# Kernel tuning notes

Measured on AMD Instinct MI355X. Metric: run time of the kernel, lower is better.

## Reference

```python
import jax, jax.numpy as jnp
import numpy as np

B, S, K, D = 2, 2048, 8, 1024
P, KP, DFF = 32, 4, 4096


def setup_inputs() -> dict:
    key = jax.random.key(0)
    ks = jax.random.split(key, 17)
    s = 0.02
    return {
        "x": jax.random.normal(ks[0], (B, S, D), jnp.float32),
        "router_out": jax.random.normal(ks[1], (B, S, D), jnp.float32),
        "topk_neuron_idx": jax.random.randint(ks[2], (B, S, K), 0, 512, jnp.int32),
        "topk_neuron_weights": jax.random.uniform(ks[3], (B, S, K), jnp.float32),
        "selected_neurons": jax.random.normal(ks[4], (B, S, K, D), jnp.float32),
        "context": jax.random.normal(ks[5], (B, S, D), jnp.float32),
        "Wq": jax.random.normal(ks[6], (D, D), jnp.float32) * s,
        "bq": jnp.zeros((D,), jnp.float32),
        "Wk": jax.random.normal(ks[7], (D, D), jnp.float32) * s,
        "bk": jnp.zeros((D,), jnp.float32),
        "Wv": jax.random.normal(ks[8], (D, D), jnp.float32) * s,
        "bv": jnp.zeros((D,), jnp.float32),
        "pattern_queries": jax.random.normal(ks[9], (P, D), jnp.float32) * s,
        "Wup": jax.random.normal(ks[10], (DFF, D), jnp.float32) * s,
        "bup": jnp.zeros((DFF,), jnp.float32),
        "Wdown": jax.random.normal(ks[11], (D, DFF), jnp.float32) * s,
        "bdown": jnp.zeros((D,), jnp.float32),
    }


def reference(x, router_out, topk_neuron_idx, topk_neuron_weights,
              selected_neurons, context, Wq, bq, Wk, bk, Wv, bv,
              pattern_queries, Wup, bup, Wdown, bdown):
    scale = 1.0 / jnp.sqrt(jnp.float32(D))
    # K-wide neuron self-attention (per token), torch Linear: y = x @ W.T + b
    q = jnp.einsum('bskd,ed->bske', selected_neurons, Wq) + bq
    kk = jnp.einsum('bskd,ed->bske', selected_neurons, Wk) + bk
    v = jnp.einsum('bskd,ed->bske', selected_neurons, Wv) + bv
    attn = jax.nn.softmax(jnp.einsum('bsqd,bskd->bsqk', q, kk) * scale, axis=-1)
    interacted = jnp.einsum('bsqk,bskd->bsqd', attn, v)  # [B,S,K,D]
    # pattern similarity: [B,S,P,K]
    nps = jnp.einsum('pd,bskd->bspk', pattern_queries, interacted) * scale
    neuron_based = (nps * topk_neuron_weights[:, :, None, :]).sum(-1)  # [B,S,P]
    context_based = jnp.einsum('bsd,pd->bsp', context, pattern_queries)
    pattern_scores = 0.5 * neuron_based + 0.5 * context_based
    topk_scores, topk_idx = jax.lax.top_k(pattern_scores, KP)  # [B,S,KP]
    topk_w = jax.nn.softmax(topk_scores, axis=-1)
    sel_attn = jnp.take_along_axis(nps, topk_idx[..., None], axis=2)  # [B,S,KP,K]
    final_attn = (topk_w[..., None] * jax.nn.softmax(sel_attn, axis=-1)).sum(2)  # [B,S,K]
    aggregated = jnp.einsum('bsk,bskd->bsd', final_attn, interacted)
    combined = x + aggregated
    h = jax.nn.gelu(combined @ Wup.T + bup, approximate=False)
    return h @ Wdown.T + bdown
```

## Files before the change

### kernel.cpp

```cpp
#include <hip/hip_runtime.h>
#include <math.h>

typedef unsigned short ushort_t;
typedef __attribute__((ext_vector_type(8))) short short8;
typedef __attribute__((ext_vector_type(4))) float floatx4;

static __device__ __forceinline__ ushort_t f2bf(float f){
  unsigned int u = __float_as_uint(f);
  unsigned int r = u + 0x7FFFu + ((u >> 16) & 1u);
  return (ushort_t)(r >> 16);
}
static __device__ __forceinline__ void unpack8(uint4 u, float* f){
  f[0] = __uint_as_float(u.x << 16); f[1] = __uint_as_float(u.x & 0xffff0000u);
  f[2] = __uint_as_float(u.y << 16); f[3] = __uint_as_float(u.y & 0xffff0000u);
  f[4] = __uint_as_float(u.z << 16); f[5] = __uint_as_float(u.z & 0xffff0000u);
  f[6] = __uint_as_float(u.w << 16); f[7] = __uint_as_float(u.w & 0xffff0000u);
}
static __device__ __forceinline__ uint4 pack8(const float* f){
  uint4 u;
  u.x = (unsigned)f2bf(f[0]) | ((unsigned)f2bf(f[1]) << 16);
  u.y = (unsigned)f2bf(f[2]) | ((unsigned)f2bf(f[3]) << 16);
  u.z = (unsigned)f2bf(f[4]) | ((unsigned)f2bf(f[5]) << 16);
  u.w = (unsigned)f2bf(f[6]) | ((unsigned)f2bf(f[7]) << 16);
  return u;
}

static __device__ __forceinline__ void gload16(const void* g, void* l){
  __builtin_amdgcn_global_load_lds((const __attribute__((address_space(1))) void*)g,
                                   (__attribute__((address_space(3))) void*)l, 16, 0, 0);
}

static __device__ __forceinline__ float gelu_f(float v){
  float w = v * (-1.5957691216f - 0.0713548162f * v * v);
  return v / (1.0f + __expf(w));
}

__global__ __launch_bounds__(256) void k_cvt_multi(
    const float* __restrict__ s0, ushort_t* __restrict__ d0, int e0,
    const float* __restrict__ s1, ushort_t* __restrict__ d1, int e1,
    const float* __restrict__ s2, ushort_t* __restrict__ d2, int e2,
    const float* __restrict__ s3, ushort_t* __restrict__ d3, int e3,
    const float* __restrict__ s4, ushort_t* __restrict__ d4, int e4,
    const float* __restrict__ s5, ushort_t* __restrict__ d5, int e5){
  int i = blockIdx.x * 256 + threadIdx.x;
  const float* s; ushort_t* d; int b;
  if      (i < e0){ s = s0; d = d0; b = 0;  }
  else if (i < e1){ s = s1; d = d1; b = e0; }
  else if (i < e2){ s = s2; d = d2; b = e1; }
  else if (i < e3){ s = s3; d = d3; b = e2; }
  else if (i < e4){ s = s4; d = d4; b = e3; }
  else if (i < e5){ s = s5; d = d5; b = e4; }
  else return;
  int j = i - b;
  float4 v = ((const float4*)s)[j];
  unsigned long long p = (unsigned long long)f2bf(v.x)
                       | ((unsigned long long)f2bf(v.y) << 16)
                       | ((unsigned long long)f2bf(v.z) << 32)
                       | ((unsigned long long)f2bf(v.w) << 48);
  ((unsigned long long*)d)[j] = p;
}

__global__ __launch_bounds__(256) void k_transpose3(const float* __restrict__ s0, ushort_t* __restrict__ d0,
                                                    const float* __restrict__ s1, ushort_t* __restrict__ d1,
                                                    const float* __restrict__ s2, ushort_t* __restrict__ d2){
  __shared__ float tile[32][33];
  const float* in; ushort_t* out;
  if      (blockIdx.z == 0){ in = s0; out = d0; }
  else if (blockIdx.z == 1){ in = s1; out = d1; }
  else                     { in = s2; out = d2; }
  int bx = blockIdx.x * 32, by = blockIdx.y * 32;
  int tx = threadIdx.x & 31, ty = threadIdx.x >> 5;
  for (int i = 0; i < 32; i += 8)
    tile[ty + i][tx] = in[(size_t)(by + ty + i) * 1024 + bx + tx];
  __syncthreads();
  for (int i = 0; i < 32; i += 8)
    out[(size_t)(bx + ty + i) * 1024 + by + tx] = f2bf(tile[tx][ty + i]);
}

__global__ __launch_bounds__(256) void k_prep(const float* __restrict__ bq,
                                              const ushort_t* __restrict__ WKT,
                                              float* __restrict__ wv,
                                              const float* __restrict__ pat,
                                              const float* __restrict__ bv,
                                              float* __restrict__ pb,
                                              const ushort_t* __restrict__ WVT,
                                              const ushort_t* __restrict__ PATB,
                                              ushort_t* __restrict__ PVB,
                                              const ushort_t* __restrict__ CTXB,
                                              float* __restrict__ CBb){
  __shared__ ushort_t As[128 * 32];
  __shared__ ushort_t Bs[32 * 32];
  const int bid = blockIdx.x;
  const int l = threadIdx.x & 63;
  if (bid < 256){
    int d = (bid << 2) + (threadIdx.x >> 6);
    const uint4* row = (const uint4*)(WKT + (size_t)d * 1024 + (l << 4));
    const float4* b4 = (const float4*)(bq + (l << 4));
    float w[16], bb[16];
    unpack8(row[0], w); unpack8(row[1], w + 8);
#pragma unroll
    for (int i = 0; i < 4; i++){
      float4 v = b4[i];
      bb[i*4] = v.x; bb[i*4+1] = v.y; bb[i*4+2] = v.z; bb[i*4+3] = v.w;
    }
    float a = 0.f;
#pragma unroll
    for (int i = 0; i < 16; i++) a += w[i] * bb[i];
#pragma unroll
    for (int s = 1; s < 64; s <<= 1) a += __shfl_xor(a, s);
    if (l == 0) wv[d] = a;
  } else if (bid < 264){
    int p = ((bid - 256) << 2) + (threadIdx.x >> 6);
    const float4* pr = (const float4*)(pat + p * 1024) + l;
    const float4* b4 = (const float4*)bv + l;
    float a = 0.f;
#pragma unroll
    for (int i = 0; i < 4; i++){
      float4 x = pr[i * 64], y = b4[i * 64];
      a += x.x * y.x + x.y * y.y + x.z * y.z + x.w * y.w;
    }
#pragma unroll
    for (int s = 1; s < 64; s <<= 1) a += __shfl_xor(a, s);
    if (l == 0) pb[p] = a;
  } else if (bid < 520){
    int d = ((bid - 264) << 2) + (threadIdx.x >> 6);
    const uint4* wr = (const uint4*)(WVT + (size_t)d * 1024 + (l << 4));
    float w[16];
    unpack8(wr[0], w); unpack8(wr[1], w + 8);
    for (int p = 0; p < 32; p++){
      const uint4* pr = (const uint4*)(PATB + p * 1024 + (l << 4));
      float pw[16];
      unpack8(pr[0], pw); unpack8(pr[1], pw + 8);
      float a = 0.f;
#pragma unroll
      for (int i = 0; i < 16; i++) a += w[i] * pw[i];
#pragma unroll
      for (int s = 1; s < 64; s <<= 1) a += __shfl_xor(a, s);
      if (l == 0) PVB[p * 1024 + d] = f2bf(a);
    }
  } else {
    const int tid = threadIdx.x;
    const int w = tid >> 6;
    const int m0 = (bid - 520) << 7;
    const int rA = (w << 4) + (l >> 2);
    const int cA = (l & 3) << 3;
    const int fr = l & 15, fq = l >> 4;
    const int K = 1024;
    floatx4 acc[2][2];
#pragma unroll
    for (int i = 0; i < 2; i++)
#pragma unroll
      for (int j = 0; j < 2; j++) acc[i][j] = (floatx4)0.0f;
    const ushort_t* Ab = CTXB + (size_t)(m0 + rA) * K + cA;
    const ushort_t* Bb = PATB + (size_t)rA * K + cA;
    const size_t row64 = (size_t)64 * K;
    for (int k0 = 0; k0 < K; k0 += 32){
      __syncthreads();
      gload16(Ab + k0, As + (w << 9));
      gload16(Ab + row64 + k0, As + 2048 + (w << 9));
      if (w < 2) gload16(Bb + k0, Bs + (w << 9));
      __syncthreads();
      short8 af[2], bg[2];
#pragma unroll
      for (int i = 0; i < 2; i++)
        af[i] = *(const short8*)(As + (((w << 5) + (i << 4) + fr) << 5) + (fq << 3));
#pragma unroll
      for (int j = 0; j < 2; j++)
        bg[j] = *(const short8*)(Bs + (((j << 4) + fr) << 5) + (fq << 3));
#pragma unroll
      for (int i = 0; i < 2; i++)
#pragma unroll
        for (int j = 0; j < 2; j++)
          acc[i][j] = __builtin_amdgcn_mfma_f32_16x16x32_bf16(af[i], bg[j], acc[i][j], 0, 0, 0);
    }
#pragma unroll
    for (int i = 0; i < 2; i++){
      int row = m0 + (w << 5) + (i << 4) + (fq << 2);
#pragma unroll
      for (int j = 0; j < 2; j++){
        int col = (j << 4) + fr;
#pragma unroll
        for (int r = 0; r < 4; r++)
          CBb[(size_t)(row + r) * 32 + col] = acc[i][j][r];
      }
    }
  }
}

template<int MODE, int GN, int NG>
__global__ __launch_bounds__(256) void k_gemm_bt(const ushort_t* __restrict__ A,
                                                 const ushort_t* __restrict__ B,
                                                 void* __restrict__ C,
                                                 const float* __restrict__ bias,
                                                 const float* __restrict__ Xadd,
                                                 int N, int K){
  __shared__ ushort_t As[2 * 128 * 32];
  __shared__ ushort_t Bs[2 * 128 * 32];
  const int tid = threadIdx.x;
  const int w = tid >> 6, l = tid & 63;
  const int id = blockIdx.x;
  const int xcd = id & 7;
  const int t2 = id >> 3;
  const int nmq = (int)(gridDim.x >> 3) / GN;
  const int gsz = nmq * NG;
  const int g = t2 / gsz, r = t2 - g * gsz;
  const int mq = r / NG, nw = r - mq * NG;
  const int nt = g * NG + nw;
  const int mt = (mq << 3) + xcd;
  const int m0 = mt << 7, n0 = nt << 7;
  const int wm = (w >> 1) << 6, wn = (w & 1) << 6;
  const int rA = (w << 4) + (l >> 2);
  const int cA = (l & 3) << 3;
  const int fr = l & 15, fq = l >> 4;

  floatx4 acc[4][4];
#pragma unroll
  for (int i = 0; i < 4; i++)
#pragma unroll
    for (int j = 0; j < 4; j++) acc[i][j] = (floatx4)0.0f;

  const ushort_t* Ab = A + (size_t)(m0 + rA) * K + cA;
  const ushort_t* Bb = B + (size_t)(n0 + rA) * K + cA;
  const size_t row64 = (size_t)64 * K;
  ushort_t* Asw = As + (w << 9);
  ushort_t* Bsw = Bs + (w << 9);

  for (int k0 = 0; k0 < K; k0 += 64){
    __syncthreads();
    gload16(Ab + k0, Asw);
    gload16(Ab + row64 + k0, Asw + 2048);
    gload16(Ab + k0 + 32, Asw + 4096);
    gload16(Ab + row64 + k0 + 32, Asw + 6144);
    gload16(Bb + k0, Bsw);
    gload16(Bb + row64 + k0, Bsw + 2048);
    gload16(Bb + k0 + 32, Bsw + 4096);
    gload16(Bb + row64 + k0 + 32, Bsw + 6144);
    __syncthreads();
#pragma unroll
    for (int h = 0; h < 2; h++){
      const ushort_t* Ah = As + (h << 12);
      const ushort_t* Bh = Bs + (h << 12);
      short8 af[4], bg[4];
#pragma unroll
      for (int i = 0; i < 4; i++){
        af[i] = *(const short8*)(Ah + ((wm + (i << 4) + fr) << 5) + (fq << 3));
        bg[i] = *(const short8*)(Bh + ((wn + (i << 4) + fr) << 5) + (fq << 3));
      }
#pragma unroll
      for (int i = 0; i < 4; i++)
#pragma unroll
        for (int j = 0; j < 4; j++)
          acc[i][j] = __builtin_amdgcn_mfma_f32_16x16x32_bf16(af[i], bg[j], acc[i][j], 0, 0, 0);
    }
  }

#pragma unroll
  for (int i = 0; i < 4; i++){
    int row = m0 + wm + (i << 4) + (fq << 2);
#pragma unroll
    for (int j = 0; j < 4; j++){
      int col = n0 + wn + (j << 4) + fr;
      float b = (MODE >= 1) ? bias[col] : 0.0f;
#pragma unroll
      for (int r2 = 0; r2 < 4; r2++){
        float v = acc[i][j][r2] + b;
        size_t idx = (size_t)(row + r2) * N + col;
        if (MODE == 2) v += Xadd[idx];
        if (MODE == 3) v = gelu_f(v);
        if (MODE == 4) ((float*)C)[idx] = v;
        else           ((ushort_t*)C)[idx] = f2bf(v);
      }
    }
  }
}

template<int MODE, int GN>
__global__ __launch_bounds__(256) void k_gemm_bt64(const ushort_t* __restrict__ A,
                                                   const ushort_t* __restrict__ B,
                                                   void* __restrict__ C,
                                                   const float* __restrict__ bias,
                                                   const float* __restrict__ Xadd,
                                                   int N, int K){
  __shared__ ushort_t As[2 * 64 * 32];
  __shared__ ushort_t Bs[2 * 128 * 32];
  const int tid = threadIdx.x;
  const int w = tid >> 6, l = tid & 63;
  const int id = blockIdx.x;
  const int xcd = id & 7;
  const int t2 = id >> 3;
  const int nmq = (int)(gridDim.x >> 3) / GN;
  const int nt = t2 / nmq;
  const int mq = t2 - nt * nmq;
  const int mt = (mq << 3) + xcd;
  const int m0 = mt << 6, n0 = nt << 7;
  const int wm = (w >> 1) << 5, wn = (w & 1) << 6;
  const int rA = (w << 4) + (l >> 2);
  const int cA = (l & 3) << 3;
  const int fr = l & 15, fq = l >> 4;

  floatx4 acc[2][4];
#pragma unroll
  for (int i = 0; i < 2; i++)
#pragma unroll
    for (int j = 0; j < 4; j++) acc[i][j] = (floatx4)0.0f;

  const ushort_t* Ab = A + (size_t)(m0 + rA) * K + cA;
  const ushort_t* Bb = B + (size_t)(n0 + rA) * K + cA;
  const size_t row64 = (size_t)64 * K;

  for (int k0 = 0; k0 < K; k0 += 64){
    __syncthreads();
    gload16(Ab + k0, As + (w << 9));
    gload16(Ab + k0 + 32, As + 2048 + (w << 9));
    gload16(Bb + k0, Bs + (w << 9));
    gload16(Bb + row64 + k0, Bs + 2048 + (w << 9));
    gload16(Bb + k0 + 32, Bs + 4096 + (w << 9));
    gload16(Bb + row64 + k0 + 32, Bs + 6144 + (w << 9));
    __syncthreads();
#pragma unroll
    for (int h = 0; h < 2; h++){
      const ushort_t* Ah = As + (h << 11);
      const ushort_t* Bh = Bs + (h << 12);
      short8 af[2], bg[4];
#pragma unroll
      for (int i = 0; i < 2; i++)
        af[i] = *(const short8*)(Ah + ((wm + (i << 4) + fr) << 5) + (fq << 3));
#pragma unroll
      for (int j = 0; j < 4; j++)
        bg[j] = *(const short8*)(Bh + ((wn + (j << 4) + fr) << 5) + (fq << 3));
#pragma unroll
      for (int i = 0; i < 2; i++)
#pragma unroll
        for (int j = 0; j < 4; j++)
          acc[i][j] = __builtin_amdgcn_mfma_f32_16x16x32_bf16(af[i], bg[j], acc[i][j], 0, 0, 0);
    }
  }

#pragma unroll
  for (int i = 0; i < 2; i++){
    int row = m0 + wm + (i << 4) + (fq << 2);
#pragma unroll
    for (int j = 0; j < 4; j++){
      int col = n0 + wn + (j << 4) + fr;
      float b = (MODE >= 2) ? bias[col] : 0.0f;
#pragma unroll
      for (int r = 0; r < 4; r++){
        float v = acc[i][j][r] + b;
        size_t idx = (size_t)(row + r) * N + col;
        if (MODE == 2) v += Xadd[idx];
        if (MODE == 4) ((float*)C)[idx] = v;
        else           ((ushort_t*)C)[idx] = f2bf(v);
      }
    }
  }
}

__global__ __launch_bounds__(256) void k_attn(const ushort_t* __restrict__ T,
                                              const ushort_t* __restrict__ SNB,
                                              const ushort_t* __restrict__ PVB,
                                              const float* __restrict__ PBv,
                                              const float* __restrict__ CB,
                                              const float* __restrict__ TW,
                                              ushort_t* __restrict__ GSN){
  __shared__ float logit_s[4 * 256];
  __shared__ float attn_s[8 * 64];
  __shared__ float npr_s[8 * 256];
  __shared__ float nps_s[8 * 256];
  __shared__ float sc_s[8 * 32];
  __shared__ float tw_s[8 * 8];
  __shared__ float pb_s[32];
  __shared__ int   sel_s[8 * 4];
  __shared__ float tkw_s[8 * 4], rmax_s[8 * 4], rsum_s[8 * 4], fa_s[8 * 8], g_s[8 * 8];

  const int t = threadIdx.x;
  const int w = t >> 6, l = t & 63;
  const int tok0 = blockIdx.x << 3;
  const int pair = (blockIdx.x << 2) + w;

  {
    const size_t rbase = (size_t)pair * 16 + (l & 15);
    const int ko = (l >> 4) << 3;
    const ushort_t* Ap = T   + rbase * 1024 + ko;
    const ushort_t* Bp = SNB + rbase * 1024 + ko;
    const ushort_t* P0 = PVB + (size_t)(l & 15) * 1024 + ko;
    const ushort_t* P1 = P0 + 16 * 1024;
    floatx4 aL = (floatx4)0.0f, aP0 = (floatx4)0.0f, aP1 = (floatx4)0.0f;
#pragma unroll 4
    for (int k0 = 0; k0 < 1024; k0 += 32){
      short8 b = *(const short8*)(Bp + k0);
      aL  = __builtin_amdgcn_mfma_f32_16x16x32_bf16(*(const short8*)(Ap + k0), b, aL, 0, 0, 0);
      aP0 = __builtin_amdgcn_mfma_f32_16x16x32_bf16(*(const short8*)(P0 + k0), b, aP0, 0, 0, 0);
      aP1 = __builtin_amdgcn_mfma_f32_16x16x32_bf16(*(const short8*)(P1 + k0), b, aP1, 0, 0, 0);
    }
    const int col = l & 15, r0 = (l >> 4) << 2;
#pragma unroll
    for (int r = 0; r < 4; r++)
      logit_s[(w << 8) + (r0 + r) * 16 + col] = aL[r] * 0.03125f;
    const int tokloc = (w << 1) + (col >> 3), kk = col & 7;
#pragma unroll
    for (int r = 0; r < 4; r++){
      npr_s[(tokloc << 8) + kk * 32 + (r0 + r)]      = aP0[r];
      npr_s[(tokloc << 8) + kk * 32 + (r0 + r) + 16] = aP1[r];
    }
  }
  if (t < 64) tw_s[t] = TW[(tok0 << 3) + t];
  if (t < 32) pb_s[t] = PBv[t];
  __syncthreads();

  const int loc = t >> 5, q = t & 31;
  if (q < 8){
    const float* lrow = logit_s + ((loc >> 1) << 8) + (loc & 1) * 136 + q * 16;
    float a[8]; float m = -1e30f;
#pragma unroll
    for (int j = 0; j < 8; j++){ a[j] = lrow[j]; m = fmaxf(m, a[j]); }
    float s = 0.f;
#pragma unroll
    for (int j = 0; j < 8; j++){ a[j] = expf(a[j] - m); s += a[j]; }
    float inv = 1.f / s;
#pragma unroll
    for (int j = 0; j < 8; j++) attn_s[(loc << 6) + q * 8 + j] = a[j] * inv;
  }
  __syncthreads();

  {
    const int qq = q & 7, p0 = (q >> 3) << 3;
    float a[8];
#pragma unroll
    for (int k = 0; k < 8; k++) a[k] = attn_s[(loc << 6) + qq * 8 + k];
    const float* np = npr_s + (loc << 8);
    float* npsr = nps_s + (loc << 8);
    for (int p = p0; p < p0 + 8; p++){
      float acc = pb_s[p];
#pragma unroll
      for (int k = 0; k < 8; k++) acc += a[k] * np[k * 32 + p];
      npsr[p * 8 + qq] = acc * 0.03125f;
    }
  }
  __syncthreads();

  {
    const float* npsr = nps_s + (loc << 8);
    float nb = 0.f;
#pragma unroll
    for (int qq = 0; qq < 8; qq++) nb += npsr[q * 8 + qq] * tw_s[(loc << 3) + qq];
    sc_s[(loc << 5) + q] = 0.5f * nb + 0.5f * CB[((size_t)(tok0 + loc) << 5) + q];
  }
  __syncthreads();

  if (q == 0){
    const float* sc = sc_s + (loc << 5);
    unsigned used = 0; float vals[4]; int idx[4];
    for (int kp = 0; kp < 4; kp++){
      float best = -1e30f; int bi = 0;
      for (int p = 0; p < 32; p++)
        if (!((used >> p) & 1u) && sc[p] > best){ best = sc[p]; bi = p; }
      used |= 1u << bi; vals[kp] = best; idx[kp] = bi;
    }
    float mm = vals[0], ss = 0.f, e[4];
    for (int kp = 0; kp < 4; kp++){ e[kp] = expf(vals[kp] - mm); ss += e[kp]; }
    for (int kp = 0; kp < 4; kp++){ tkw_s[(loc << 2) + kp] = e[kp] / ss; sel_s[(loc << 2) + kp] = idx[kp]; }
  }
  __syncthreads();

  if (q < 4){
    const float* npsr = nps_s + (loc << 8);
    int p = sel_s[(loc << 2) + q];
    float mm = -1e30f;
    for (int j = 0; j < 8; j++) mm = fmaxf(mm, npsr[p * 8 + j]);
    float ss = 0.f;
    for (int j = 0; j < 8; j++) ss += expf(npsr[p * 8 + j] - mm);
    rmax_s[(loc << 2) + q] = mm; rsum_s[(loc << 2) + q] = ss;
  }
  __syncthreads();

  if (q < 8){
    const float* npsr = nps_s + (loc << 8);
    float f = 0.f;
    for (int kp = 0; kp < 4; kp++){
      int p = sel_s[(loc << 2) + kp];
      f += tkw_s[(loc << 2) + kp] * expf(npsr[p * 8 + q] - rmax_s[(loc << 2) + kp]) / rsum_s[(loc << 2) + kp];
    }
    fa_s[(loc << 3) + q] = f;
  }
  __syncthreads();

  if (q < 8){
    float g = 0.f;
    for (int qq = 0; qq < 8; qq++) g += fa_s[(loc << 3) + qq] * attn_s[(loc << 6) + qq * 8 + q];
    g_s[(loc << 3) + q] = g;
  }
  __syncthreads();

  for (int tl = 0; tl < 2; tl++){
    const int tkl = (w << 1) + tl;
    const size_t tok = (size_t)tok0 + tkl;
    float o[16];
#pragma unroll
    for (int i = 0; i < 16; i++) o[i] = 0.f;
#pragma unroll
    for (int k = 0; k < 8; k++){
      float gk = g_s[(tkl << 3) + k];
      const uint4* src = (const uint4*)(SNB + ((tok << 3) + k) * 1024 + (l << 4));
      float f0[8], f1[8];
      unpack8(src[0], f0);
      unpack8(src[1], f1);
#pragma unroll
      for (int i = 0; i < 8; i++){ o[i] += gk * f0[i]; o[8 + i] += gk * f1[i]; }
    }
    uint4* dst = (uint4*)(GSN + tok * 1024 + (l << 4));
    dst[0] = pack8(o);
    dst[1] = pack8(o + 8);
  }
}

extern "C" void kernel_launch(void* const* d_in, const int* in_sizes, int n_in,
                              void* d_out, int out_size, void* d_ws, size_t ws_size,
                              hipStream_t stream){
  (void)in_sizes; (void)n_in; (void)out_size; (void)ws_size;
  const float* x   = (const float*)d_in[0];
  const float* tw  = (const float*)d_in[3];
  const float* SN  = (const float*)d_in[4];
  const float* ctx = (const float*)d_in[5];
  const float* Wq  = (const float*)d_in[6];
  const float* bq  = (const float*)d_in[7];
  const float* Wk  = (const float*)d_in[8];
  const float* Wv  = (const float*)d_in[10];
  const float* bv  = (const float*)d_in[11];
  const float* pat = (const float*)d_in[12];
  const float* Wup = (const float*)d_in[13];
  const float* bup = (const float*)d_in[14];
  const float* Wdn = (const float*)d_in[15];
  const float* bdn = (const float*)d_in[16];
  float* out = (float*)d_out;

  char* ws = (char*)d_ws;
  size_t off = 0;
  auto alloc = [&](size_t bytes) -> char* {
    char* p = ws + off;
    off = (off + bytes + 255) & ~(size_t)255;
    return p;
  };
  ushort_t* SNB  = (ushort_t*)alloc(67108864);
  ushort_t* TB   = (ushort_t*)alloc(67108864);
  float*    CBb  = (float*)alloc(524288);
  ushort_t* GSN  = (ushort_t*)alloc(8388608);
  ushort_t* CTXB = (ushort_t*)alloc(8388608);
  ushort_t* PATB = (ushort_t*)alloc(65536);
  ushort_t* WVB  = (ushort_t*)alloc(2097152);
  ushort_t* WUPB = (ushort_t*)alloc(8388608);
  ushort_t* WDNB = (ushort_t*)alloc(8388608);
  ushort_t* ATB  = (ushort_t*)alloc(2097152);
  ushort_t* WKTB = (ushort_t*)alloc(2097152);
  ushort_t* WQTB = (ushort_t*)alloc(2097152);
  ushort_t* WVTB = (ushort_t*)alloc(2097152);
  ushort_t* PVB  = (ushort_t*)alloc(65536);
  float*    WVEC = (float*)alloc(4096);
  float*    PBv  = (float*)alloc(128);
  ushort_t* H    = SNB;
  ushort_t* CMB  = TB;

  const int e0 = 8388608, e1 = e0 + 1048576, e2 = e1 + 8192,
            e3 = e2 + 262144, e4 = e3 + 1048576, e5 = e4 + 1048576;
  k_cvt_multi<<<(e5 + 255) / 256, 256, 0, stream>>>(
      SN, SNB, e0, ctx, CTXB, e1, pat, PATB, e2,
      Wv, WVB, e3, Wup, WUPB, e4, Wdn, WDNB, e5);
  k_transpose3<<<dim3(32, 32, 3), 256, 0, stream>>>(Wq, WQTB, Wk, WKTB, Wv, WVTB);
  k_prep<<<552, 256, 0, stream>>>(bq, WKTB, WVEC, pat, bv, PBv, WVTB, PATB, PVB, CTXB, CBb);

  k_gemm_bt64<0, 8><<<128, 256, 0, stream>>>(WKTB, WQTB, ATB, nullptr, nullptr, 1024, 1024);
  k_gemm_bt<1, 8, 8><<<2048, 256, 0, stream>>>(SNB, ATB, TB, WVEC, nullptr, 1024, 1024);
  k_attn<<<512, 256, 0, stream>>>(TB, SNB, PVB, PBv, CBb, tw, GSN);
  k_gemm_bt64<2, 8><<<512, 256, 0, stream>>>(GSN, WVB, CMB, bv, x, 1024, 1024);
  k_gemm_bt<3, 32, 4><<<1024, 256, 0, stream>>>(CMB, WUPB, H, bup, nullptr, 4096, 1024);
  k_gemm_bt64<4, 8><<<512, 256, 0, stream>>>(H, WDNB, out, bdn, nullptr, 1024, 4096);
}
```

Measured before the change: 587.2 us.

## Replace 128x128 GEMM with 256x256 8-wave pipelined kernel using swizzled LDS

Replaces the 128x128-tile, 4-wave bf16 GEMM with a 256x256-tile, 8-wave kernel. It double-buffers 64-wide K slices in XOR-swizzled LDS and interleaves staged global loads with four quadrant MFMA phases, using explicit waitcnt, barriers, sched_barrier and setprio. This targets the two large GEMMs (neuron projection and up-projection with GELU), aiming to raise MFMA utilisation, cut LDS bank conflicts and overlap memory traffic with compute. The cost is much larger LDS use (128 KB per block), fewer blocks, and fragile hand-tuned wait counts.

```diff
diff --git a/kernel.cpp b/kernel.cpp
--- a/kernel.cpp
+++ b/kernel.cpp
@@ -187,91 +187,147 @@
   }
 }
 
-template<int MODE, int GN, int NG>
-__global__ __launch_bounds__(256) void k_gemm_bt(const ushort_t* __restrict__ A,
-                                                 const ushort_t* __restrict__ B,
-                                                 void* __restrict__ C,
-                                                 const float* __restrict__ bias,
-                                                 const float* __restrict__ Xadd,
-                                                 int N, int K){
-  __shared__ ushort_t As[2 * 128 * 32];
-  __shared__ ushort_t Bs[2 * 128 * 32];
+#define SBAR_  __builtin_amdgcn_s_barrier()
+#define SCHED_ __builtin_amdgcn_sched_barrier(0)
+#define LGKM0_ asm volatile("s_waitcnt lgkmcnt(0)" ::: "memory")
+#define VM4_   asm volatile("s_waitcnt vmcnt(4)" ::: "memory")
+#define VM2_   asm volatile("s_waitcnt vmcnt(2)" ::: "memory")
+#define VM0_   asm volatile("s_waitcnt vmcnt(0)" ::: "memory")
+
+#define STG_(Gp, Lp, qh, tt) do{ \
+    const ushort_t* _g = (Gp) + (size_t)(((qh) << 7) + (wid << 3)) * K + ((tt) << 6); \
+    char* _l = (Lp) + ((((tt) & 1) << 15) | ((qh) << 14) | (wid << 10)); \
+    gload16(_g, _l); \
+    gload16(_g + ((size_t)K << 6), _l + 8192); \
+  }while(0)
+
+#define RDA_(qm, cb) do{ \
+    _Pragma("unroll") \
+    for (int _i = 0; _i < 4; _i++){ \
+      af[_i][0] = *(const short8*)(AsB + (cb) + ((qm) << 14) + arow + (_i << 11) + c0); \
+      af[_i][1] = *(const short8*)(AsB + (cb) + ((qm) << 14) + arow + (_i << 11) + c1); \
+    } }while(0)
+
+#define RDB_(qn, cb) do{ \
+    _Pragma("unroll") \
+    for (int _j = 0; _j < 2; _j++){ \
+      bg[qn][_j][0] = *(const short8*)(BsB + (cb) + ((qn) << 14) + brow + (_j << 11) + c0); \
+      bg[qn][_j][1] = *(const short8*)(BsB + (cb) + ((qn) << 14) + brow + (_j << 11) + c1); \
+    } }while(0)
+
+#define MFMA_(qm, qn) do{ \
+    _Pragma("unroll") \
+    for (int _i = 0; _i < 4; _i++) \
+    _Pragma("unroll") \
+      for (int _j = 0; _j < 2; _j++){ \
+        acc[qm][_i][qn][_j] = __builtin_amdgcn_mfma_f32_16x16x32_bf16(af[_i][0], bg[qn][_j][0], acc[qm][_i][qn][_j], 0, 0, 0); \
+        acc[qm][_i][qn][_j] = __builtin_amdgcn_mfma_f32_16x16x32_bf16(af[_i][1], bg[qn][_j][1], acc[qm][_i][qn][_j], 0, 0, 0); \
+      } }while(0)
+
+template<int MODE>
+__global__ __launch_bounds__(512, 2) void k_gemm8(const ushort_t* __restrict__ A,
+                                                  const ushort_t* __restrict__ B,
+                                                  void* __restrict__ C,
+                                                  const float* __restrict__ bias,
+                                                  int N, int K, int ntn){
+  __shared__ __align__(16) ushort_t As[2 * 256 * 64];
+  __shared__ __align__(16) ushort_t Bs[2 * 256 * 64];
   const int tid = threadIdx.x;
-  const int w = tid >> 6, l = tid & 63;
+  const int wid = tid >> 6, l = tid & 63;
+  const int wr = wid >> 2, wc = wid & 3;
+  const int fr = l & 15, fq = l >> 4;
   const int id = blockIdx.x;
-  const int xcd = id & 7;
-  const int t2 = id >> 3;
-  const int nmq = (int)(gridDim.x >> 3) / GN;
-  const int gsz = nmq * NG;
-  const int g = t2 / gsz, r = t2 - g * gsz;
-  const int mq = r / NG, nw = r - mq * NG;
-  const int nt = g * NG + nw;
+  const int xcd = id & 7, t2 = id >> 3;
+  const int nt = t2 % ntn, mq = t2 / ntn;
   const int mt = (mq << 3) + xcd;
-  const int m0 = mt << 7, n0 = nt << 7;
-  const int wm = (w >> 1) << 6, wn = (w & 1) << 6;
-  const int rA = (w << 4) + (l >> 2);
-  const int cA = (l & 3) << 3;
-  const int fr = l & 15, fq = l >> 4;
-
-  floatx4 acc[4][4];
-#pragma unroll
-  for (int i = 0; i < 4; i++)
-#pragma unroll
-    for (int j = 0; j < 4; j++) acc[i][j] = (floatx4)0.0f;
-
-  const ushort_t* Ab = A + (size_t)(m0 + rA) * K + cA;
-  const ushort_t* Bb = B + (size_t)(n0 + rA) * K + cA;
-  const size_t row64 = (size_t)64 * K;
-  ushort_t* Asw = As + (w << 9);
-  ushort_t* Bsw = Bs + (w << 9);
-
-  for (int k0 = 0; k0 < K; k0 += 64){
-    __syncthreads();
-    gload16(Ab + k0, Asw);
-    gload16(Ab + row64 + k0, Asw + 2048);
-    gload16(Ab + k0 + 32, Asw + 4096);
-    gload16(Ab + row64 + k0 + 32, Asw + 6144);
-    gload16(Bb + k0, Bsw);
-    gload16(Bb + row64 + k0, Bsw + 2048);
-    gload16(Bb + k0 + 32, Bsw + 4096);
-    gload16(Bb + row64 + k0 + 32, Bsw + 6144);
-    __syncthreads();
-#pragma unroll
-    for (int h = 0; h < 2; h++){
-      const ushort_t* Ah = As + (h << 12);
-      const ushort_t* Bh = Bs + (h << 12);
-      short8 af[4], bg[4];
-#pragma unroll
-      for (int i = 0; i < 4; i++){
-        af[i] = *(const short8*)(Ah + ((wm + (i << 4) + fr) << 5) + (fq << 3));
-        bg[i] = *(const short8*)(Bh + ((wn + (i << 4) + fr) << 5) + (fq << 3));
-      }
-#pragma unroll
-      for (int i = 0; i < 4; i++)
-#pragma unroll
-        for (int j = 0; j < 4; j++)
-          acc[i][j] = __builtin_amdgcn_mfma_f32_16x16x32_bf16(af[i], bg[j], acc[i][j], 0, 0, 0);
-    }
-  }
-
-#pragma unroll
-  for (int i = 0; i < 4; i++){
-    int row = m0 + wm + (i << 4) + (fq << 2);
-#pragma unroll
-    for (int j = 0; j < 4; j++){
-      int col = n0 + wn + (j << 4) + fr;
-      float b = (MODE >= 1) ? bias[col] : 0.0f;
-#pragma unroll
-      for (int r2 = 0; r2 < 4; r2++){
-        float v = acc[i][j][r2] + b;
-        size_t idx = (size_t)(row + r2) * N + col;
-        if (MODE == 2) v += Xadd[idx];
-        if (MODE == 3) v = gelu_f(v);
-        if (MODE == 4) ((float*)C)[idx] = v;
-        else           ((ushort_t*)C)[idx] = f2bf(v);
-      }
-    }
-  }
+  const int m0 = mt << 8, n0 = nt << 8;
+  const int NT = K >> 6;
+
+  const int sgr = l >> 3;
+  const int sgc = ((l & 7) ^ (l >> 3)) << 3;
+  const ushort_t* Ag = A + (size_t)(m0 + sgr) * K + sgc;
+  const ushort_t* Bg = B + (size_t)(n0 + sgr) * K + sgc;
+  char* AsB = (char*)As;
+  char* BsB = (char*)Bs;
+  const int c0 = ((fq ^ (fr & 7)) << 4);
+  const int c1 = (((4 | fq) ^ (fr & 7)) << 4);
+  const int arow = (wr << 13) + fr * 128;
+  const int brow = (wc << 12) + fr * 128;
+
+  floatx4 acc[2][4][2][2];
+#pragma unroll
+  for (int a = 0; a < 2; a++)
+#pragma unroll
+    for (int b = 0; b < 4; b++)
+#pragma unroll
+      for (int c = 0; c < 2; c++)
+#pragma unroll
+        for (int d = 0; d < 2; d++) acc[a][b][c][d] = (floatx4)0.0f;
+  short8 af[4][2], bg[2][2][2];
+
+  STG_(Ag, AsB, 0, 0);
+  STG_(Bg, BsB, 0, 0);
+  STG_(Bg, BsB, 1, 0);
+  STG_(Ag, AsB, 1, 0);
+  VM4_; SBAR_;
+
+  for (int t = 0; t < NT - 1; t++){
+    const int cur = (t & 1) << 15;
+    const int tn = t + 1;
+    RDA_(0, cur); RDB_(0, cur);
+    STG_(Ag, AsB, 0, tn);
+    SCHED_; SBAR_; LGKM0_; SCHED_;
+    __builtin_amdgcn_s_setprio(1); MFMA_(0, 0); __builtin_amdgcn_s_setprio(0);
+    SCHED_; VM4_; SBAR_;
+    RDB_(1, cur);
+    STG_(Bg, BsB, 0, tn);
+    SCHED_; SBAR_; LGKM0_; SCHED_;
+    __builtin_amdgcn_s_setprio(1); MFMA_(0, 1); __builtin_amdgcn_s_setprio(0);
+    SCHED_; VM4_; SBAR_;
+    RDA_(1, cur);
+    STG_(Bg, BsB, 1, tn);
+    SCHED_; SBAR_; LGKM0_; SCHED_;
+    __builtin_amdgcn_s_setprio(1); MFMA_(1, 1); __builtin_amdgcn_s_setprio(0);
+    SCHED_; SBAR_;
+    STG_(Ag, AsB, 1, tn);
+    SCHED_; SBAR_; SCHED_;
+    __builtin_amdgcn_s_setprio(1); MFMA_(1, 0); __builtin_amdgcn_s_setprio(0);
+    SCHED_; VM4_; SBAR_;
+  }
+  {
+    const int cur = ((NT - 1) & 1) << 15;
+    RDA_(0, cur); RDB_(0, cur);
+    SCHED_; SBAR_; LGKM0_; SCHED_;
+    __builtin_amdgcn_s_setprio(1); MFMA_(0, 0); __builtin_amdgcn_s_setprio(0);
+    SCHED_; VM2_; SBAR_;
+    RDB_(1, cur);
+    SCHED_; SBAR_; LGKM0_; SCHED_;
+    __builtin_amdgcn_s_setprio(1); MFMA_(0, 1); __builtin_amdgcn_s_setprio(0);
+    SCHED_; VM0_; SBAR_;
+    RDA_(1, cur);
+    SCHED_; SBAR_; LGKM0_; SCHED_;
+    __builtin_amdgcn_s_setprio(1); MFMA_(1, 1); MFMA_(1, 0); __builtin_amdgcn_s_setprio(0);
+  }
+
+#pragma unroll
+  for (int qm = 0; qm < 2; qm++)
+#pragma unroll
+    for (int i = 0; i < 4; i++){
+      const int row = m0 + (qm << 7) + (wr << 6) + (i << 4) + (fq << 2);
+#pragma unroll
+      for (int qn = 0; qn < 2; qn++)
+#pragma unroll
+        for (int j = 0; j < 2; j++){
+          const int col = n0 + (qn << 7) + (wc << 5) + (j << 4) + fr;
+          const float bsv = bias[col];
+#pragma unroll
+          for (int r = 0; r < 4; r++){
+            float v = acc[qm][i][qn][j][r] + bsv;
+            if (MODE == 3) v = gelu_f(v);
+            ((ushort_t*)C)[(size_t)(row + r) * N + col] = f2bf(v);
+          }
+        }
+    }
 }
 
 template<int MODE, int GN>
@@ -568,9 +624,9 @@
   k_prep<<<552, 256, 0, stream>>>(bq, WKTB, WVEC, pat, bv, PBv, WVTB, PATB, PVB, CTXB, CBb);
 
   k_gemm_bt64<0, 8><<<128, 256, 0, stream>>>(WKTB, WQTB, ATB, nullptr, nullptr, 1024, 1024);
-  k_gemm_bt<1, 8, 8><<<2048, 256, 0, stream>>>(SNB, ATB, TB, WVEC, nullptr, 1024, 1024);
+  k_gemm8<1><<<512, 512, 0, stream>>>(SNB, ATB, TB, WVEC, 1024, 1024, 4);
   k_attn<<<512, 256, 0, stream>>>(TB, SNB, PVB, PBv, CBb, tw, GSN);
   k_gemm_bt64<2, 8><<<512, 256, 0, stream>>>(GSN, WVB, CMB, bv, x, 1024, 1024);
-  k_gemm_bt<3, 32, 4><<<1024, 256, 0, stream>>>(CMB, WUPB, H, bup, nullptr, 4096, 1024);
+  k_gemm8<3><<<256, 512, 0, stream>>>(CMB, WUPB, H, bup, 4096, 1024, 16);
   k_gemm_bt64<4, 8><<<512, 256, 0, stream>>>(H, WDNB, out, bdn, nullptr, 1024, 4096);
 }
```

New measurement: 557.9 us. -5.0%, faster.
